# Performance work log

Hardware: AMD Instinct MI355X
Metric: run time of the kernel (lower is better)

## Reference

```python
import jax, jax.numpy as jnp
import numpy as np

N, H, C, K = 8192, 1024, 1024, 32  # tokens, nhid, ncls, words-per-class (vocab = C*K = 32768)
R = 0.1  # init_weights uniform range


def setup_inputs() -> dict:
    key = jax.random.key(0)
    k0, k1, k2, k3 = jax.random.split(key, 4)
    x = jax.random.normal(k0, (N, H), jnp.float32)
    cls = jax.random.randint(k1, (N,), 0, C)  # per-token class id (derived from word2cls[target])
    W_cls = jax.random.uniform(k2, (C, H), jnp.float32, -R, R)
    b_cls = jnp.zeros((C,), jnp.float32)
    W_words = jax.random.uniform(k3, (C, K, H), jnp.float32, -R, R)  # stacked per-class Linear weights
    b_words = jnp.zeros((C, K), jnp.float32)
    return {"x": x, "cls": cls, "W_cls": W_cls, "b_cls": b_cls,
            "W_words": W_words, "b_words": b_words}


def reference(x, cls, W_cls, b_cls, W_words, b_words):
    # Class head: nn.Linear(nhid, ncls) over all tokens -> [N, C]
    p_class = x @ W_cls.T + b_cls
    # Per-class word heads: original gathers tokens per class (index_select) and
    # applies that class's nn.Linear(nhid, K). Equivalent grouped form: gather each
    # token's class weights and do a batched matvec. p_words[i] are the within-class
    # logits of token i under class cls[i] (same math, token order instead of
    # dict-of-classes order).
    Wg = W_words[cls]                                   # [N, K, H]
    p_words = jnp.einsum('nh,nkh->nk', x, Wg) + b_words[cls]  # [N, K]
    return p_class, p_words
```

## Files before the change

kernel.cpp:

```cpp
#include <hip/hip_runtime.h>
#include <stdint.h>

#define HDIM 1024
#define CDIM 1024
#define KW   32
#define CAP  64

typedef unsigned short u16;
typedef __attribute__((ext_vector_type(8))) short bf16x8;
typedef __attribute__((ext_vector_type(4))) float f32x4;

#define GLDS16(gp, lp)                                                                    \
  __builtin_amdgcn_global_load_lds((const __attribute__((address_space(1))) void*)(gp),   \
                                   (__attribute__((address_space(3))) void*)(lp), 16, 0, 0)

#define WAITV(N) asm volatile("s_waitcnt vmcnt(" #N ")" ::: "memory")

__device__ __forceinline__ u16 f2bf(float f) {
  union { float f; unsigned u; } v; v.f = f;
  unsigned r = v.u + 0x7FFFu + ((v.u >> 16) & 1u);
  return (u16)(r >> 16);
}

__device__ __forceinline__ bf16x8 pack8(float4 a, float4 b) {
  bf16x8 r;
  r[0] = (short)f2bf(a.x); r[1] = (short)f2bf(a.y);
  r[2] = (short)f2bf(a.z); r[3] = (short)f2bf(a.w);
  r[4] = (short)f2bf(b.x); r[5] = (short)f2bf(b.y);
  r[6] = (short)f2bf(b.z); r[7] = (short)f2bf(b.w);
  return r;
}

__global__ __launch_bounds__(256) void convert_and_zero(const float* __restrict__ x,
                                                        u16* __restrict__ xbf, int n4x,
                                                        const float* __restrict__ Wc,
                                                        u16* __restrict__ wbf, int n4w,
                                                        int* __restrict__ cursor) {
  const int tid0 = blockIdx.x * 256 + threadIdx.x;
  if (tid0 < CDIM) cursor[tid0] = 0;
  const int total = n4x + n4w;
  const int stride = gridDim.x * 256;
  for (int j = tid0; j < total; j += stride) {
    float4 v;
    if (j < n4x) v = ((const float4*)x)[j];
    else         v = ((const float4*)Wc)[j - n4x];
    ushort4 o;
    o.x = f2bf(v.x); o.y = f2bf(v.y); o.z = f2bf(v.z); o.w = f2bf(v.w);
    if (j < n4x) ((ushort4*)xbf)[j] = o;
    else         ((ushort4*)wbf)[j - n4x] = o;
  }
}

__global__ __launch_bounds__(256) void scatter_kernel(const int* __restrict__ cls, int N,
                                                      int* __restrict__ cursor,
                                                      int* __restrict__ toklist) {
  const int i = blockIdx.x * 256 + threadIdx.x;
  if (i < N) {
    const int c = cls[i];
    const int pos = atomicAdd(&cursor[c], 1);
    if (pos < CAP) toklist[c * CAP + pos] = i;
  }
}

#define STAGE_P(PA, PB, KT)                    \
  GLDS16(xb + ga0 + (KT), (PA) + c0 * 8);      \
  GLDS16(xb + ga1 + (KT), (PA) + c1 * 8);      \
  GLDS16(wb + gb0 + (KT), (PB) + c0 * 8);      \
  GLDS16(wb + gb1 + (KT), (PB) + c1 * 8);

#define COMPUTE_P(PA, PB)                                                                    \
  {                                                                                          \
    bf16x8 a[4], b[4];                                                                       \
    _Pragma("unroll") for (int m = 0; m < 4; m++)                                            \
      a[m] = *(const bf16x8*)&(PA)[(wr * 64 + m * 16 + fr) * 32 + koff];                     \
    _Pragma("unroll") for (int n = 0; n < 4; n++)                                            \
      b[n] = *(const bf16x8*)&(PB)[(wc * 64 + n * 16 + fr) * 32 + koff];                     \
    _Pragma("unroll") for (int m = 0; m < 4; m++)                                            \
      _Pragma("unroll") for (int n = 0; n < 4; n++)                                          \
        acc[m][n] = __builtin_amdgcn_mfma_f32_16x16x32_bf16(a[m], b[n], acc[m][n], 0, 0, 0); \
  }

__device__ __forceinline__ void gemm_block(int gid, char* smem,
                                           const u16* __restrict__ xb,
                                           const u16* __restrict__ wb,
                                           const float* __restrict__ bcls,
                                           float* __restrict__ out) {
  u16* As = (u16*)smem;
  u16* Bs = (u16*)smem + 3 * 4096;
  const int tid  = threadIdx.x;
  const int lane = tid & 63;
  const int wid  = tid >> 6;
  const int wr   = wid >> 1, wc = wid & 1;
  const int bm = gid >> 3, bn = gid & 7;

  const int c0 = tid, c1 = tid + 256;
  const size_t ga0 = (size_t)(bm * 128 + (c0 >> 2)) * HDIM + (c0 & 3) * 8;
  const size_t ga1 = (size_t)(bm * 128 + (c1 >> 2)) * HDIM + (c1 & 3) * 8;
  const size_t gb0 = (size_t)(bn * 128 + (c0 >> 2)) * HDIM + (c0 & 3) * 8;
  const size_t gb1 = (size_t)(bn * 128 + (c1 >> 2)) * HDIM + (c1 & 3) * 8;

  f32x4 acc[4][4] = {};
  const int fr   = lane & 15;
  const int koff = (lane >> 4) * 8;

  const int ccol = lane & 15;
  float bias[4];
#pragma unroll
  for (int n = 0; n < 4; n++) bias[n] = bcls[bn * 128 + wc * 64 + n * 16 + ccol];
  WAITV(0);

  u16 *A0 = As, *A1 = As + 4096, *A2 = As + 8192;
  u16 *B0 = Bs, *B1 = Bs + 4096, *B2 = Bs + 8192;
  STAGE_P(A0, B0, 0);
  STAGE_P(A1, B1, 32);

  for (int kt = 0; kt < HDIM; kt += 32) {
    if (kt + 64 < HDIM) {
      STAGE_P(A2, B2, kt + 64);
      WAITV(8);
    } else if (kt + 32 < HDIM) {
      WAITV(4);
    } else {
      WAITV(0);
    }
    __builtin_amdgcn_s_barrier();
    __builtin_amdgcn_sched_barrier(0);
    __builtin_amdgcn_s_setprio(1);
    COMPUTE_P(A0, B0);
    __builtin_amdgcn_s_setprio(0);
    __builtin_amdgcn_sched_barrier(0);
    __builtin_amdgcn_s_barrier();
    u16* t;
    t = A0; A0 = A1; A1 = A2; A2 = t;
    t = B0; B0 = B1; B1 = B2; B2 = t;
  }

  const int crow = (lane >> 4) * 4;
#pragma unroll
  for (int n = 0; n < 4; n++) {
    const int col = bn * 128 + wc * 64 + n * 16 + ccol;
#pragma unroll
    for (int m = 0; m < 4; m++) {
      const int row0 = bm * 128 + wr * 64 + m * 16 + crow;
#pragma unroll
      for (int r = 0; r < 4; r++)
        out[(size_t)(row0 + r) * CDIM + col] = acc[m][n][r] + bias[n];
    }
  }
}

__device__ __forceinline__ void words_block(int c, char* smem,
                                            const u16* __restrict__ xbf,
                                            const float* __restrict__ Ww,
                                            const float* __restrict__ bw,
                                            const int* __restrict__ toklist,
                                            const int* __restrict__ cursor,
                                            float* __restrict__ outw) {
  const int count = min(cursor[c], CAP);
  if (count <= 0) return;
  float* red = (float*)smem;
  int* toks  = (int*)(smem + 8192);
  const int tid  = threadIdx.x;
  const int lane = tid & 63, wave = tid >> 6;
  const int fr   = lane & 15;
  const int koff = (lane >> 4) * 8;
  const float* Wc = Ww + (size_t)c * KW * HDIM;
  const int k0 = wave * 256;

  for (int base = 0; base < count; base += 16) {
    const int nt = min(16, count - base);
    __syncthreads();
    if (tid < 16) toks[tid] = toklist[c * CAP + base + min(tid, nt - 1)];
    __syncthreads();
    const u16* arow = xbf + (size_t)toks[fr] * HDIM;
    const float* b0row = Wc + (size_t)fr * HDIM;
    const float* b1row = Wc + (size_t)(16 + fr) * HDIM;
    f32x4 acc0 = {}, acc1 = {};
#pragma unroll
    for (int ks = 0; ks < 8; ks++) {
      const int kt = k0 + ks * 32 + koff;
      bf16x8 a = *(const bf16x8*)(arow + kt);
      float4 b0a = *(const float4*)(b0row + kt);
      float4 b0b = *(const float4*)(b0row + kt + 4);
      float4 b1a = *(const float4*)(b1row + kt);
      float4 b1b = *(const float4*)(b1row + kt + 4);
      bf16x8 b0 = pack8(b0a, b0b);
      bf16x8 b1 = pack8(b1a, b1b);
      acc0 = __builtin_amdgcn_mfma_f32_16x16x32_bf16(a, b0, acc0, 0, 0, 0);
      acc1 = __builtin_amdgcn_mfma_f32_16x16x32_bf16(a, b1, acc1, 0, 0, 0);
    }
    const int rb = (lane >> 4) * 4, cc = lane & 15;
#pragma unroll
    for (int r = 0; r < 4; r++) {
      red[((wave * 2 + 0) * 16 + rb + r) * 16 + cc] = acc0[r];
      red[((wave * 2 + 1) * 16 + rb + r) * 16 + cc] = acc1[r];
    }
    __syncthreads();
    const int row = tid >> 4, col = tid & 15;
#pragma unroll
    for (int wcx = 0; wcx < 2; wcx++) {
      float s = 0.f;
#pragma unroll
      for (int w = 0; w < 4; w++) s += red[((w * 2 + wcx) * 16 + row) * 16 + col];
      if (row < nt) {
        const int word = wcx * 16 + col;
        outw[(size_t)toks[row] * KW + word] = s + bw[c * KW + word];
      }
    }
  }
}

__global__ __launch_bounds__(256) void mega_kernel(const u16* __restrict__ xbf,
                                                   const u16* __restrict__ wbf,
                                                   const float* __restrict__ bc,
                                                   float* __restrict__ out,
                                                   const float* __restrict__ Ww,
                                                   const float* __restrict__ bw,
                                                   const int* __restrict__ toklist,
                                                   const int* __restrict__ cursor,
                                                   float* __restrict__ outw, int nbg) {
  __shared__ __align__(16) char smem[49216];
  const int bid = blockIdx.x;
  if (2 * nbg == CDIM) {
    if (bid % 3 == 0) gemm_block(bid / 3, smem, xbf, wbf, bc, out);
    else              words_block(bid - bid / 3 - 1, smem, xbf, Ww, bw, toklist, cursor, outw);
  } else {
    if (bid < nbg) gemm_block(bid, smem, xbf, wbf, bc, out);
    else           words_block(bid - nbg, smem, xbf, Ww, bw, toklist, cursor, outw);
  }
}

__global__ __launch_bounds__(256) void words_kernel(const float* __restrict__ x,
                                                    const int* __restrict__ cls,
                                                    const float* __restrict__ Ww,
                                                    const float* __restrict__ bw,
                                                    float* __restrict__ outw) {
  const int n    = blockIdx.x;
  const int c    = cls[n];
  const int lane = threadIdx.x & 63;
  const int wave = threadIdx.x >> 6;
  const float4* xr = (const float4*)(x + (size_t)n * HDIM);
  float4 xv[4];
#pragma unroll
  for (int i = 0; i < 4; i++) xv[i] = xr[lane + 64 * i];
  const float* Wc = Ww + (size_t)c * KW * HDIM;
#pragma unroll
  for (int wi = 0; wi < 8; wi++) {
    const int w = wave * 8 + wi;
    const float4* wrp = (const float4*)(Wc + (size_t)w * HDIM);
    float s = 0.f;
#pragma unroll
    for (int i = 0; i < 4; i++) {
      float4 wv = wrp[lane + 64 * i];
      s += xv[i].x * wv.x + xv[i].y * wv.y + xv[i].z * wv.z + xv[i].w * wv.w;
    }
#pragma unroll
    for (int off = 32; off > 0; off >>= 1) s += __shfl_down(s, off);
    if (lane == 0) outw[(size_t)n * KW + w] = s + bw[c * KW + w];
  }
}

__global__ __launch_bounds__(256) void gemm_f32_naive(const float* __restrict__ x,
                                                      const float* __restrict__ Wc,
                                                      const float* __restrict__ bc,
                                                      float* __restrict__ out) {
  __shared__ float xs[HDIM];
  const int n = blockIdx.x;
  const int tid = threadIdx.x;
  ((float4*)xs)[tid] = ((const float4*)(x + (size_t)n * HDIM))[tid];
  __syncthreads();
  for (int c = tid; c < CDIM; c += 256) {
    const float* wr = Wc + (size_t)c * HDIM;
    float s = 0.f;
    for (int h = 0; h < HDIM; h += 4) {
      float4 wv = *(const float4*)(wr + h);
      s += xs[h] * wv.x + xs[h + 1] * wv.y + xs[h + 2] * wv.z + xs[h + 3] * wv.w;
    }
    out[(size_t)n * CDIM + c] = s + bc[c];
  }
}

extern "C" void kernel_launch(void* const* d_in, const int* in_sizes, int n_in,
                              void* d_out, int out_size, void* d_ws, size_t ws_size,
                              hipStream_t stream) {
  const float* x   = (const float*)d_in[0];
  const int*   cls = (const int*)d_in[1];
  const float* Wc  = (const float*)d_in[2];
  const float* bc  = (const float*)d_in[3];
  const float* Ww  = (const float*)d_in[4];
  const float* bw  = (const float*)d_in[5];
  float* out = (float*)d_out;
  const int N = in_sizes[0] / HDIM;
  float* outw = out + (size_t)N * CDIM;

  const size_t bf_bytes  = ((size_t)N * HDIM + (size_t)CDIM * HDIM) * sizeof(u16);
  const size_t ints_off  = (bf_bytes + 63) & ~(size_t)63;
  const size_t need_all  = ints_off + ((size_t)CDIM + (size_t)CDIM * CAP) * sizeof(int);

  if (ws_size >= need_all && (N % 128) == 0) {
    u16* xbf = (u16*)d_ws;
    u16* wbf = xbf + (size_t)N * HDIM;
    int* cursor  = (int*)((char*)d_ws + ints_off);
    int* toklist = cursor + CDIM;

    convert_and_zero<<<2048, 256, 0, stream>>>(x, xbf, N * HDIM / 4,
                                               Wc, wbf, CDIM * HDIM / 4, cursor);
    scatter_kernel<<<(N + 255) / 256, 256, 0, stream>>>(cls, N, cursor, toklist);
    const int nbg = (N / 128) * (CDIM / 128);
    mega_kernel<<<nbg + CDIM, 256, 0, stream>>>(xbf, wbf, bc, out, Ww, bw,
                                                toklist, cursor, outw, nbg);
  } else {
    gemm_f32_naive<<<N, 256, 0, stream>>>(x, Wc, bc, out);
    words_kernel<<<N, 256, 0, stream>>>(x, cls, Ww, bw, outw);
  }
}
```

Measured before the change: 75.38 us.

## Split mega kernel into 256x128 GEMM with swizzled LDS and separate words kernel

Replaces the fused mega kernel, which interleaved GEMM and word-head blocks, with two launches. The GEMM now uses 512-thread blocks over 256x128 tiles, each holding 8 waves. An XOR swizzle on the LDS layout avoids bank conflicts on the MFMA fragment reads. The word-head computation runs as its own kernel afterwards. This raises A/B reuse per block and removes bank conflicts, but loses the overlap between the words work and the GEMM and adds a kernel launch.

```diff
diff --git a/kernel.cpp b/kernel.cpp
--- a/kernel.cpp
+++ b/kernel.cpp
@@ -65,43 +65,52 @@
 #define STAGE_P(PA, PB, KT)                    \
   GLDS16(xb + ga0 + (KT), (PA) + c0 * 8);      \
   GLDS16(xb + ga1 + (KT), (PA) + c1 * 8);      \
-  GLDS16(wb + gb0 + (KT), (PB) + c0 * 8);      \
-  GLDS16(wb + gb1 + (KT), (PB) + c1 * 8);
+  GLDS16(wb + gb2 + (KT), (PB) + c2 * 8);
 
 #define COMPUTE_P(PA, PB)                                                                    \
   {                                                                                          \
     bf16x8 a[4], b[4];                                                                       \
     _Pragma("unroll") for (int m = 0; m < 4; m++)                                            \
-      a[m] = *(const bf16x8*)&(PA)[(wr * 64 + m * 16 + fr) * 32 + koff];                     \
+      a[m] = *(const bf16x8*)&(PA)[aoff[m]];                                                 \
     _Pragma("unroll") for (int n = 0; n < 4; n++)                                            \
-      b[n] = *(const bf16x8*)&(PB)[(wc * 64 + n * 16 + fr) * 32 + koff];                     \
+      b[n] = *(const bf16x8*)&(PB)[boff[n]];                                                 \
     _Pragma("unroll") for (int m = 0; m < 4; m++)                                            \
       _Pragma("unroll") for (int n = 0; n < 4; n++)                                          \
         acc[m][n] = __builtin_amdgcn_mfma_f32_16x16x32_bf16(a[m], b[n], acc[m][n], 0, 0, 0); \
   }
 
-__device__ __forceinline__ void gemm_block(int gid, char* smem,
-                                           const u16* __restrict__ xb,
-                                           const u16* __restrict__ wb,
-                                           const float* __restrict__ bcls,
-                                           float* __restrict__ out) {
-  u16* As = (u16*)smem;
-  u16* Bs = (u16*)smem + 3 * 4096;
+__global__ __launch_bounds__(512, 4) void gemm_bf16_kernel(const u16* __restrict__ xb,
+                                                           const u16* __restrict__ wb,
+                                                           const float* __restrict__ bcls,
+                                                           float* __restrict__ out) {
+  __shared__ u16 As_s[3 * 256 * 32];
+  __shared__ u16 Bs_s[3 * 128 * 32];
   const int tid  = threadIdx.x;
   const int lane = tid & 63;
   const int wid  = tid >> 6;
   const int wr   = wid >> 1, wc = wid & 1;
-  const int bm = gid >> 3, bn = gid & 7;
-
-  const int c0 = tid, c1 = tid + 256;
-  const size_t ga0 = (size_t)(bm * 128 + (c0 >> 2)) * HDIM + (c0 & 3) * 8;
-  const size_t ga1 = (size_t)(bm * 128 + (c1 >> 2)) * HDIM + (c1 & 3) * 8;
-  const size_t gb0 = (size_t)(bn * 128 + (c0 >> 2)) * HDIM + (c0 & 3) * 8;
-  const size_t gb1 = (size_t)(bn * 128 + (c1 >> 2)) * HDIM + (c1 & 3) * 8;
+  const int bm = blockIdx.x >> 3, bn = blockIdx.x & 7;
+
+  const int c0 = tid, c1 = tid + 512, c2 = tid;
+  const size_t ga0 = (size_t)(bm * 256 + (c0 >> 2)) * HDIM + (((c0 & 3) ^ ((c0 >> 3) & 3)) * 8);
+  const size_t ga1 = (size_t)(bm * 256 + (c1 >> 2)) * HDIM + (((c1 & 3) ^ ((c1 >> 3) & 3)) * 8);
+  const size_t gb2 = (size_t)(bn * 128 + (c2 >> 2)) * HDIM + (((c2 & 3) ^ ((c2 >> 3) & 3)) * 8);
 
   f32x4 acc[4][4] = {};
-  const int fr   = lane & 15;
-  const int koff = (lane >> 4) * 8;
+  const int fr = lane & 15;
+  const int kx = lane >> 4;
+
+  int aoff[4], boff[4];
+#pragma unroll
+  for (int m = 0; m < 4; m++) {
+    const int R = wr * 64 + m * 16 + fr;
+    aoff[m] = R * 32 + ((kx ^ ((R >> 1) & 3)) << 3);
+  }
+#pragma unroll
+  for (int n = 0; n < 4; n++) {
+    const int R = wc * 64 + n * 16 + fr;
+    boff[n] = R * 32 + ((kx ^ ((R >> 1) & 3)) << 3);
+  }
 
   const int ccol = lane & 15;
   float bias[4];
@@ -109,17 +118,17 @@
   for (int n = 0; n < 4; n++) bias[n] = bcls[bn * 128 + wc * 64 + n * 16 + ccol];
   WAITV(0);
 
-  u16 *A0 = As, *A1 = As + 4096, *A2 = As + 8192;
-  u16 *B0 = Bs, *B1 = Bs + 4096, *B2 = Bs + 8192;
+  u16 *A0 = As_s, *A1 = As_s + 8192, *A2 = As_s + 16384;
+  u16 *B0 = Bs_s, *B1 = Bs_s + 4096, *B2 = Bs_s + 8192;
   STAGE_P(A0, B0, 0);
   STAGE_P(A1, B1, 32);
 
   for (int kt = 0; kt < HDIM; kt += 32) {
     if (kt + 64 < HDIM) {
       STAGE_P(A2, B2, kt + 64);
-      WAITV(8);
+      WAITV(6);
     } else if (kt + 32 < HDIM) {
-      WAITV(4);
+      WAITV(3);
     } else {
       WAITV(0);
     }
@@ -141,7 +150,7 @@
     const int col = bn * 128 + wc * 64 + n * 16 + ccol;
 #pragma unroll
     for (int m = 0; m < 4; m++) {
-      const int row0 = bm * 128 + wr * 64 + m * 16 + crow;
+      const int row0 = bm * 256 + wr * 64 + m * 16 + crow;
 #pragma unroll
       for (int r = 0; r < 4; r++)
         out[(size_t)(row0 + r) * CDIM + col] = acc[m][n][r] + bias[n];
@@ -149,17 +158,17 @@
   }
 }
 
-__device__ __forceinline__ void words_block(int c, char* smem,
-                                            const u16* __restrict__ xbf,
-                                            const float* __restrict__ Ww,
-                                            const float* __restrict__ bw,
-                                            const int* __restrict__ toklist,
-                                            const int* __restrict__ cursor,
-                                            float* __restrict__ outw) {
+__global__ __launch_bounds__(256) void words_mfma(const u16* __restrict__ xbf,
+                                                  const float* __restrict__ Ww,
+                                                  const float* __restrict__ bw,
+                                                  const int* __restrict__ toklist,
+                                                  const int* __restrict__ cursor,
+                                                  float* __restrict__ outw) {
+  const int c = blockIdx.x;
   const int count = min(cursor[c], CAP);
   if (count <= 0) return;
-  float* red = (float*)smem;
-  int* toks  = (int*)(smem + 8192);
+  __shared__ float red[4][2][16][16];
+  __shared__ int toks[16];
   const int tid  = threadIdx.x;
   const int lane = tid & 63, wave = tid >> 6;
   const int fr   = lane & 15;
@@ -192,8 +201,8 @@
     const int rb = (lane >> 4) * 4, cc = lane & 15;
 #pragma unroll
     for (int r = 0; r < 4; r++) {
-      red[((wave * 2 + 0) * 16 + rb + r) * 16 + cc] = acc0[r];
-      red[((wave * 2 + 1) * 16 + rb + r) * 16 + cc] = acc1[r];
+      red[wave][0][rb + r][cc] = acc0[r];
+      red[wave][1][rb + r][cc] = acc1[r];
     }
     __syncthreads();
     const int row = tid >> 4, col = tid & 15;
@@ -201,32 +210,12 @@
     for (int wcx = 0; wcx < 2; wcx++) {
       float s = 0.f;
 #pragma unroll
-      for (int w = 0; w < 4; w++) s += red[((w * 2 + wcx) * 16 + row) * 16 + col];
+      for (int w = 0; w < 4; w++) s += red[w][wcx][row][col];
       if (row < nt) {
         const int word = wcx * 16 + col;
         outw[(size_t)toks[row] * KW + word] = s + bw[c * KW + word];
       }
     }
-  }
-}
-
-__global__ __launch_bounds__(256) void mega_kernel(const u16* __restrict__ xbf,
-                                                   const u16* __restrict__ wbf,
-                                                   const float* __restrict__ bc,
-                                                   float* __restrict__ out,
-                                                   const float* __restrict__ Ww,
-                                                   const float* __restrict__ bw,
-                                                   const int* __restrict__ toklist,
-                                                   const int* __restrict__ cursor,
-                                                   float* __restrict__ outw, int nbg) {
-  __shared__ __align__(16) char smem[49216];
-  const int bid = blockIdx.x;
-  if (2 * nbg == CDIM) {
-    if (bid % 3 == 0) gemm_block(bid / 3, smem, xbf, wbf, bc, out);
-    else              words_block(bid - bid / 3 - 1, smem, xbf, Ww, bw, toklist, cursor, outw);
-  } else {
-    if (bid < nbg) gemm_block(bid, smem, xbf, wbf, bc, out);
-    else           words_block(bid - nbg, smem, xbf, Ww, bw, toklist, cursor, outw);
   }
 }
 
@@ -297,7 +286,7 @@
   const size_t ints_off  = (bf_bytes + 63) & ~(size_t)63;
   const size_t need_all  = ints_off + ((size_t)CDIM + (size_t)CDIM * CAP) * sizeof(int);
 
-  if (ws_size >= need_all && (N % 128) == 0) {
+  if (ws_size >= need_all && (N % 256) == 0) {
     u16* xbf = (u16*)d_ws;
     u16* wbf = xbf + (size_t)N * HDIM;
     int* cursor  = (int*)((char*)d_ws + ints_off);
@@ -306,9 +295,8 @@
     convert_and_zero<<<2048, 256, 0, stream>>>(x, xbf, N * HDIM / 4,
                                                Wc, wbf, CDIM * HDIM / 4, cursor);
     scatter_kernel<<<(N + 255) / 256, 256, 0, stream>>>(cls, N, cursor, toklist);
-    const int nbg = (N / 128) * (CDIM / 128);
-    mega_kernel<<<nbg + CDIM, 256, 0, stream>>>(xbf, wbf, bc, out, Ww, bw,
-                                                toklist, cursor, outw, nbg);
+    gemm_bf16_kernel<<<(N / 256) * (CDIM / 128), 512, 0, stream>>>(xbf, wbf, bc, out);
+    words_mfma<<<CDIM, 256, 0, stream>>>(xbf, Ww, bw, toklist, cursor, outw);
   } else {
     gemm_f32_naive<<<N, 256, 0, stream>>>(x, Wc, bc, out);
     words_kernel<<<N, 256, 0, stream>>>(x, cls, Ww, bw, outw);
```

Measured after the change: 76.38 us. Within noise of the previous version (+1.3%).
